# Kernel tuning notes

Hardware: AMD Instinct MI355X
Metric: run time of the kernel (lower is better)

Reference implementation:

```python
import jax, jax.numpy as jnp
import numpy as np

N, E, M, D = 100000, 50000, 1000000, 128  # vertices, hyperedges, incidences, hidden


def setup_inputs() -> dict:
    key = jax.random.key(0)
    ks = jax.random.split(key, 9)
    v = jax.random.normal(ks[0], (N, D), dtype=jnp.float32)
    e = jax.random.normal(ks[1], (E, D), dtype=jnp.float32)
    vidx = jax.random.randint(ks[2], (M,), 0, N)
    eidx = jax.random.randint(ks[3], (M,), 0, E)
    v_reg_weight = jax.random.uniform(ks[4], (M, 1), dtype=jnp.float32)
    e_reg_weight = jax.random.uniform(ks[5], (M, 1), dtype=jnp.float32)
    v_reg_sum = jnp.ones((N, 1), dtype=jnp.float32)
    e_reg_sum = jnp.ones((E, 1), dtype=jnp.float32)
    # learned parameters
    W_v2e = jax.random.normal(ks[6], (D, D), dtype=jnp.float32)
    W_e2v = jax.random.normal(ks[7], (D, D), dtype=jnp.float32)
    b_v = jnp.zeros((D,), dtype=jnp.float32)
    b_e = jnp.zeros((D,), dtype=jnp.float32)
    v_weight = jax.random.uniform(ks[8], (N, 1), dtype=jnp.float32)  # args.v_weight
    return dict(v=v, e=e, vidx=vidx, eidx=eidx,
                v_reg_weight=v_reg_weight, e_reg_weight=e_reg_weight,
                v_reg_sum=v_reg_sum, e_reg_sum=e_reg_sum,
                W_v2e=W_v2e, W_e2v=W_e2v, b_v=b_v, b_e=b_e, v_weight=v_weight)


def reference(v, e, vidx, eidx, v_reg_weight, e_reg_weight, v_reg_sum, e_reg_sum,
              W_v2e, W_e2v, b_v, b_e, v_weight):
    # v2e: dense transform, gather by vidx, reweight, scatter_add into edges
    ve = jax.nn.relu(v @ W_v2e + b_v)                      # [N, D]
    v_out = v * v_weight * 4.0                             # v_fac = 4
    msg_ve = (ve * v_weight)[vidx] * v_reg_weight          # [M, D]
    e_out = e + jax.ops.segment_sum(msg_ve, eidx, num_segments=E)
    e_out = e_out / e_reg_sum
    # e2v: dense transform, gather by eidx, reweight, scatter_add into vertices
    ev = jax.nn.relu(e_out @ W_e2v + b_e)                  # [E, D]
    msg_ev = (ev / 3.0)[eidx] * e_reg_weight               # [M, D]
    v_out = v_out + jax.ops.segment_sum(msg_ev, vidx, num_segments=N)
    v_out = v_out / v_reg_sum
    # is_last_mod=True: no dropout
    return v_out, e_out
```

## Files before the change

kernel.cpp:

```cpp
#include <hip/hip_runtime.h>
#include <cstddef>

#define DD 128
#define PART_ELEMS 4096
#define MAXB 256
#define MAXW 512
#define WT_LD 136

typedef __attribute__((ext_vector_type(8))) short bf16x8;
typedef __attribute__((ext_vector_type(4))) float f32x4;

__device__ __forceinline__ unsigned bf16pk(float x, float y) {
    unsigned a = __float_as_uint(x);
    unsigned b = __float_as_uint(y);
    a = (a + 0x7FFFu + ((a >> 16) & 1u)) >> 16;
    b = (b + 0x7FFFu + ((b >> 16) & 1u)) >> 16;
    return a | (b << 16);
}
__device__ __forceinline__ unsigned short bf16r(float x) {
    unsigned u = __float_as_uint(x);
    return (unsigned short)((u + 0x7FFFu + ((u >> 16) & 1u)) >> 16);
}
__device__ __forceinline__ float bflo(unsigned u) { return __uint_as_float(u << 16); }
__device__ __forceinline__ float bfhi(unsigned u) { return __uint_as_float(u & 0xFFFF0000u); }

__global__ __launch_bounds__(256)
void conv_w_kernel(const float* __restrict__ W0, const float* __restrict__ W1,
                   unsigned short* __restrict__ Wt0, unsigned short* __restrict__ Wt1,
                   int* __restrict__ bcur_e, int* __restrict__ bcur_v, int e_cap, int v_cap)
{
    int idx = blockIdx.x * 256 + threadIdx.x;
    int k = idx >> 7, c = idx & 127;
    Wt0[c * 128 + k] = bf16r(W0[idx]);
    Wt1[c * 128 + k] = bf16r(W1[idx]);
    if (blockIdx.x == 0) {
        bcur_e[threadIdx.x] = threadIdx.x * e_cap;
        bcur_v[threadIdx.x] = threadIdx.x * v_cap;
    }
}

__global__ __launch_bounds__(256)
void part2_kernel(const int* __restrict__ eidx, const int* __restrict__ vidx,
                  const float* __restrict__ vrw, const float* __restrict__ erw,
                  int* __restrict__ bcur_e, int* __restrict__ bcur_v,
                  int2* __restrict__ tmp_e, int2* __restrict__ tmp_v,
                  int M, int e_shift, int v_shift, int e_bk, int v_bk)
{
    __shared__ int lcnt_e[MAXB], lbase_e[MAXB], lcnt_v[MAXB], lbase_v[MAXB];
    const int t = threadIdx.x;
    const int base = blockIdx.x * PART_ELEMS;
    const int end = min(base + PART_ELEMS, M);

    if (t < e_bk) lcnt_e[t] = 0;
    if (t < v_bk) lcnt_v[t] = 0;
    __syncthreads();
    for (int j = base + t; j < end; j += 256) {
        atomicAdd(&lcnt_e[eidx[j] >> e_shift], 1);
        atomicAdd(&lcnt_v[vidx[j] >> v_shift], 1);
    }
    __syncthreads();
    if (t < e_bk) { int c = lcnt_e[t]; lbase_e[t] = c ? atomicAdd(&bcur_e[t], c) : 0; lcnt_e[t] = 0; }
    if (t < v_bk) { int c = lcnt_v[t]; lbase_v[t] = c ? atomicAdd(&bcur_v[t], c) : 0; lcnt_v[t] = 0; }
    __syncthreads();
    for (int j = base + t; j < end; j += 256) {
        int ei = eidx[j], vi = vidx[j];
        int wqe = (int)(vrw[j] * 32767.0f + 0.5f); wqe = wqe < 32767 ? wqe : 32767;
        int wqv = (int)(erw[j] * 32767.0f + 0.5f); wqv = wqv < 32767 ? wqv : 32767;
        int be = ei >> e_shift;
        int pe = lbase_e[be] + atomicAdd(&lcnt_e[be], 1);
        tmp_e[pe] = make_int2(ei | (wqe << 17), vi);
        int bv = vi >> v_shift;
        int pv = lbase_v[bv] + atomicAdd(&lcnt_v[bv], 1);
        tmp_v[pv] = make_int2(vi | (wqv << 17), ei);
    }
}

__global__ __launch_bounds__(256)
void fine2_kernel(const int2* __restrict__ tmp_e, const int* __restrict__ bcur_e,
                  int e_cap, int e_shift, int En, int e_bk,
                  int* __restrict__ e_start, unsigned* __restrict__ e_pack,
                  const int2* __restrict__ tmp_v, const int* __restrict__ bcur_v,
                  int v_cap, int v_shift, int Nn, int v_bk,
                  int* __restrict__ v_start, unsigned* __restrict__ v_pack, int M)
{
    __shared__ int lcnt[MAXW];
    __shared__ int lstart[MAXW];
    __shared__ int sdata[256];
    __shared__ int scnt[256];
    __shared__ int spbase;

    const int t = threadIdx.x;
    const int2* tmp; const int* bcur; int cap, shift, n, nb, b;
    int* start; unsigned* pack;
    if ((int)blockIdx.x < e_bk) {
        tmp = tmp_e; bcur = bcur_e; cap = e_cap; shift = e_shift; n = En; nb = e_bk;
        start = e_start; pack = e_pack; b = blockIdx.x;
    } else {
        tmp = tmp_v; bcur = bcur_v; cap = v_cap; shift = v_shift; n = Nn; nb = v_bk;
        start = v_start; pack = v_pack; b = blockIdx.x - e_bk;
    }

    int cnt_t = (t < nb) ? (bcur[t] - t * cap) : 0;
    scnt[t] = cnt_t;
    __syncthreads();
    int xx = cnt_t;
    for (int off = 1; off < 256; off <<= 1) {
        int y = (t >= off) ? scnt[t - off] : 0;
        __syncthreads();
        xx += y;
        scnt[t] = xx;
        __syncthreads();
    }
    if (t == b) spbase = xx - cnt_t;
    if (b == nb - 1 && t == 0) start[n] = M;
    __syncthreads();
    const int pbase = spbase;

    const int d0 = b << shift;
    const int width = min(1 << shift, n - d0);
    const int tbase = b * cap;
    const int nrec = bcur[b] - tbase;

    lcnt[t] = 0; lcnt[t + 256] = 0;
    __syncthreads();
    for (int j = t; j < nrec; j += 256)
        atomicAdd(&lcnt[(tmp[tbase + j].x & 0x1FFFF) - d0], 1);
    __syncthreads();
    int a = lcnt[2 * t], bb = lcnt[2 * t + 1];
    int s = a + bb;
    sdata[t] = s;
    __syncthreads();
    int x = s;
    for (int off = 1; off < 256; off <<= 1) {
        int y = (t >= off) ? sdata[t - off] : 0;
        __syncthreads();
        x += y;
        sdata[t] = x;
        __syncthreads();
    }
    int ex = x - s;
    lstart[2 * t] = ex;
    lstart[2 * t + 1] = ex + a;
    lcnt[2 * t] = 0; lcnt[2 * t + 1] = 0;
    __syncthreads();
    for (int i = t; i < width; i += 256)
        start[d0 + i] = pbase + lstart[i];
    for (int j = t; j < nrec; j += 256) {
        int2 r = tmp[tbase + j];
        int di = (r.x & 0x1FFFF) - d0;
        int pos = pbase + lstart[di] + atomicAdd(&lcnt[di], 1);
        pack[pos] = (unsigned)r.y | (((unsigned)r.x >> 17) << 17);
    }
}

template<bool V2E>
__global__ __launch_bounds__(256)
void gemm_mfma_kernel(const float* __restrict__ A, const unsigned short* __restrict__ Wtg,
                      const float* __restrict__ bias, const float* __restrict__ rowwt,
                      unsigned* __restrict__ outb, int nrows, float scale)
{
    __shared__ unsigned short Wt[128 * WT_LD];
    __shared__ unsigned short At[64 * WT_LD];

    const int t = threadIdx.x;
    const int row0 = blockIdx.x * 64;

    {
        int r = t >> 1, h = t & 1;
        const uint4* src = reinterpret_cast<const uint4*>(Wtg + r * 128 + h * 64);
        uint4* dst = reinterpret_cast<uint4*>(&Wt[r * WT_LD + h * 64]);
        #pragma unroll
        for (int i = 0; i < 8; ++i) dst[i] = src[i];
    }
    {
        int r = t >> 2, q = t & 3;
        int grow = row0 + r;
        uint4 o[4];
        if (grow < nrows) {
            const float4* src = reinterpret_cast<const float4*>(A + (size_t)grow * DD + q * 32);
            #pragma unroll
            for (int i = 0; i < 4; ++i) {
                float4 f0 = src[2 * i];
                float4 f1 = src[2 * i + 1];
                o[i].x = bf16pk(f0.x, f0.y);
                o[i].y = bf16pk(f0.z, f0.w);
                o[i].z = bf16pk(f1.x, f1.y);
                o[i].w = bf16pk(f1.z, f1.w);
            }
        } else {
            #pragma unroll
            for (int i = 0; i < 4; ++i) o[i] = make_uint4(0, 0, 0, 0);
        }
        uint4* dst = reinterpret_cast<uint4*>(&At[r * WT_LD + q * 32]);
        #pragma unroll
        for (int i = 0; i < 4; ++i) dst[i] = o[i];
    }
    __syncthreads();

    const int w  = t >> 6;
    const int l  = t & 63;
    const int lr = l & 15;
    const int lk = (l >> 4) * 8;

    f32x4 acc[8];
    #pragma unroll
    for (int i = 0; i < 8; ++i) acc[i] = 0.0f;

    const int arow = w * 16 + lr;
    #pragma unroll
    for (int ks = 0; ks < 4; ++ks) {
        bf16x8 af = *reinterpret_cast<const bf16x8*>(&At[arow * WT_LD + lk + ks * 32]);
        #pragma unroll
        for (int ct = 0; ct < 8; ++ct) {
            bf16x8 bfr = *reinterpret_cast<const bf16x8*>(&Wt[(ct * 16 + lr) * WT_LD + lk + ks * 32]);
            acc[ct] = __builtin_amdgcn_mfma_f32_16x16x32_bf16(af, bfr, acc[ct], 0, 0, 0);
        }
    }

    float bcol[8];
    #pragma unroll
    for (int ct = 0; ct < 8; ++ct) bcol[ct] = bias[ct * 16 + lr];
    #pragma unroll
    for (int r = 0; r < 4; ++r) {
        int rl = w * 16 + (l >> 4) * 4 + r;
        int grow = row0 + rl;
        float rw = scale;
        if (V2E) rw = (grow < nrows) ? rowwt[grow] : 0.f;
        #pragma unroll
        for (int ct = 0; ct < 8; ++ct) {
            float val = fmaxf(acc[ct][r] + bcol[ct], 0.f) * rw;
            At[rl * WT_LD + ct * 16 + lr] = bf16r(val);
        }
    }
    {
        int r = t >> 2, part = t & 3;
        int grow = row0 + r;
        if (grow < nrows) {
            const uint4* src = reinterpret_cast<const uint4*>(&At[r * WT_LD + part * 32]);
            uint4* dst = reinterpret_cast<uint4*>(outb + (size_t)grow * 64 + part * 16);
            dst[0] = src[0]; dst[1] = src[1]; dst[2] = src[2]; dst[3] = src[3];
        }
    }
}

__global__ __launch_bounds__(256)
void e_agg_kernel(const float* __restrict__ e, const unsigned* __restrict__ vwb,
                  const int* __restrict__ start, const unsigned* __restrict__ pack,
                  const float* __restrict__ ers, float* __restrict__ eout, int E)
{
    int row = blockIdx.x * 4 + (threadIdx.x >> 6);
    if (row >= E) return;
    int lane = threadIdx.x & 63;
    int half = lane >> 5;
    int sl = lane & 31;
    int s = start[row], t = start[row + 1];

    float a0 = 0.f, a1 = 0.f, a2 = 0.f, a3 = 0.f;
    float b0 = 0.f, b1 = 0.f, b2 = 0.f, b3 = 0.f;
    float c0 = 0.f, c1 = 0.f, c2 = 0.f, c3 = 0.f;
    float d0 = 0.f, d1 = 0.f, d2 = 0.f, d3 = 0.f;

    int j = s;
    for (; j + 8 <= t; j += 8) {
        unsigned pw0 = pack[j + half];
        unsigned pw1 = pack[j + 2 + half];
        unsigned pw2 = pack[j + 4 + half];
        unsigned pw3 = pack[j + 6 + half];
        uint2 u0 = *reinterpret_cast<const uint2*>(&vwb[(size_t)(pw0 & 0x1FFFFu) * 64 + sl * 2]);
        uint2 u1 = *reinterpret_cast<const uint2*>(&vwb[(size_t)(pw1 & 0x1FFFFu) * 64 + sl * 2]);
        uint2 u2 = *reinterpret_cast<const uint2*>(&vwb[(size_t)(pw2 & 0x1FFFFu) * 64 + sl * 2]);
        uint2 u3 = *reinterpret_cast<const uint2*>(&vwb[(size_t)(pw3 & 0x1FFFFu) * 64 + sl * 2]);
        float w0 = (float)(pw0 >> 17) * (1.0f / 32767.0f);
        float w1 = (float)(pw1 >> 17) * (1.0f / 32767.0f);
        float w2 = (float)(pw2 >> 17) * (1.0f / 32767.0f);
        float w3 = (float)(pw3 >> 17) * (1.0f / 32767.0f);
        a0 = fmaf(bflo(u0.x), w0, a0); a1 = fmaf(bfhi(u0.x), w0, a1);
        a2 = fmaf(bflo(u0.y), w0, a2); a3 = fmaf(bfhi(u0.y), w0, a3);
        b0 = fmaf(bflo(u1.x), w1, b0); b1 = fmaf(bfhi(u1.x), w1, b1);
        b2 = fmaf(bflo(u1.y), w1, b2); b3 = fmaf(bfhi(u1.y), w1, b3);
        c0 = fmaf(bflo(u2.x), w2, c0); c1 = fmaf(bfhi(u2.x), w2, c1);
        c2 = fmaf(bflo(u2.y), w2, c2); c3 = fmaf(bfhi(u2.y), w2, c3);
        d0 = fmaf(bflo(u3.x), w3, d0); d1 = fmaf(bfhi(u3.x), w3, d1);
        d2 = fmaf(bflo(u3.y), w3, d2); d3 = fmaf(bfhi(u3.y), w3, d3);
    }
    for (; j < t; j += 2) {
        int jj = j + half;
        if (jj < t) {
            unsigned pw = pack[jj];
            float wm = (float)(pw >> 17) * (1.0f / 32767.0f);
            uint2 u = *reinterpret_cast<const uint2*>(&vwb[(size_t)(pw & 0x1FFFFu) * 64 + sl * 2]);
            a0 = fmaf(bflo(u.x), wm, a0); a1 = fmaf(bfhi(u.x), wm, a1);
            a2 = fmaf(bflo(u.y), wm, a2); a3 = fmaf(bfhi(u.y), wm, a3);
        }
    }
    float s0 = (a0 + b0) + (c0 + d0);
    float s1 = (a1 + b1) + (c1 + d1);
    float s2 = (a2 + b2) + (c2 + d2);
    float s3 = (a3 + b3) + (c3 + d3);
    s0 += __shfl_xor(s0, 32, 64);
    s1 += __shfl_xor(s1, 32, 64);
    s2 += __shfl_xor(s2, 32, 64);
    s3 += __shfl_xor(s3, 32, 64);
    if (half == 0) {
        float rs = 1.0f / ers[row];
        float4 er = *reinterpret_cast<const float4*>(&e[(size_t)row * DD + sl * 4]);
        float4 o = make_float4((er.x + s0) * rs, (er.y + s1) * rs,
                               (er.z + s2) * rs, (er.w + s3) * rs);
        *reinterpret_cast<float4*>(&eout[(size_t)row * DD + sl * 4]) = o;
    }
}

__global__ __launch_bounds__(256)
void v_agg_kernel(const float* __restrict__ v, const unsigned* __restrict__ evb,
                  const int* __restrict__ start, const unsigned* __restrict__ pack,
                  const float* __restrict__ vrs, const float* __restrict__ vweight,
                  float* __restrict__ vout, int N)
{
    int row = blockIdx.x * 4 + (threadIdx.x >> 6);
    if (row >= N) return;
    int lane = threadIdx.x & 63;
    int half = lane >> 5;
    int sl = lane & 31;
    int s = start[row], t = start[row + 1];

    float a0 = 0.f, a1 = 0.f, a2 = 0.f, a3 = 0.f;
    float b0 = 0.f, b1 = 0.f, b2 = 0.f, b3 = 0.f;
    float c0 = 0.f, c1 = 0.f, c2 = 0.f, c3 = 0.f;
    float d0 = 0.f, d1 = 0.f, d2 = 0.f, d3 = 0.f;

    int j = s;
    for (; j + 8 <= t; j += 8) {
        unsigned pw0 = pack[j + half];
        unsigned pw1 = pack[j + 2 + half];
        unsigned pw2 = pack[j + 4 + half];
        unsigned pw3 = pack[j + 6 + half];
        uint2 u0 = *reinterpret_cast<const uint2*>(&evb[(size_t)(pw0 & 0x1FFFFu) * 64 + sl * 2]);
        uint2 u1 = *reinterpret_cast<const uint2*>(&evb[(size_t)(pw1 & 0x1FFFFu) * 64 + sl * 2]);
        uint2 u2 = *reinterpret_cast<const uint2*>(&evb[(size_t)(pw2 & 0x1FFFFu) * 64 + sl * 2]);
        uint2 u3 = *reinterpret_cast<const uint2*>(&evb[(size_t)(pw3 & 0x1FFFFu) * 64 + sl * 2]);
        float w0 = (float)(pw0 >> 17) * (1.0f / 32767.0f);
        float w1 = (float)(pw1 >> 17) * (1.0f / 32767.0f);
        float w2 = (float)(pw2 >> 17) * (1.0f / 32767.0f);
        float w3 = (float)(pw3 >> 17) * (1.0f / 32767.0f);
        a0 = fmaf(bflo(u0.x), w0, a0); a1 = fmaf(bfhi(u0.x), w0, a1);
        a2 = fmaf(bflo(u0.y), w0, a2); a3 = fmaf(bfhi(u0.y), w0, a3);
        b0 = fmaf(bflo(u1.x), w1, b0); b1 = fmaf(bfhi(u1.x), w1, b1);
        b2 = fmaf(bflo(u1.y), w1, b2); b3 = fmaf(bfhi(u1.y), w1, b3);
        c0 = fmaf(bflo(u2.x), w2, c0); c1 = fmaf(bfhi(u2.x), w2, c1);
        c2 = fmaf(bflo(u2.y), w2, c2); c3 = fmaf(bfhi(u2.y), w2, c3);
        d0 = fmaf(bflo(u3.x), w3, d0); d1 = fmaf(bfhi(u3.x), w3, d1);
        d2 = fmaf(bflo(u3.y), w3, d2); d3 = fmaf(bfhi(u3.y), w3, d3);
    }
    for (; j < t; j += 2) {
        int jj = j + half;
        if (jj < t) {
            unsigned pw = pack[jj];
            float wm = (float)(pw >> 17) * (1.0f / 32767.0f);
            uint2 u = *reinterpret_cast<const uint2*>(&evb[(size_t)(pw & 0x1FFFFu) * 64 + sl * 2]);
            a0 = fmaf(bflo(u.x), wm, a0); a1 = fmaf(bfhi(u.x), wm, a1);
            a2 = fmaf(bflo(u.y), wm, a2); a3 = fmaf(bfhi(u.y), wm, a3);
        }
    }
    float s0 = (a0 + b0) + (c0 + d0);
    float s1 = (a1 + b1) + (c1 + d1);
    float s2 = (a2 + b2) + (c2 + d2);
    float s3 = (a3 + b3) + (c3 + d3);
    s0 += __shfl_xor(s0, 32, 64);
    s1 += __shfl_xor(s1, 32, 64);
    s2 += __shfl_xor(s2, 32, 64);
    s3 += __shfl_xor(s3, 32, 64);
    if (half == 0) {
        float rs = 1.0f / vrs[row];
        float wt = vweight[row] * 4.0f;
        float4 vr = *reinterpret_cast<const float4*>(&v[(size_t)row * DD + sl * 4]);
        float4 o = make_float4((vr.x * wt + s0) * rs, (vr.y * wt + s1) * rs,
                               (vr.z * wt + s2) * rs, (vr.w * wt + s3) * rs);
        *reinterpret_cast<float4*>(&vout[(size_t)row * DD + sl * 4]) = o;
    }
}

extern "C" void kernel_launch(void* const* d_in, const int* in_sizes, int n_in,
                              void* d_out, int out_size, void* d_ws, size_t ws_size,
                              hipStream_t stream)
{
    const float* v       = (const float*)d_in[0];
    const float* e       = (const float*)d_in[1];
    const int*   vidx    = (const int*)d_in[2];
    const int*   eidx    = (const int*)d_in[3];
    const float* vrw     = (const float*)d_in[4];
    const float* erw     = (const float*)d_in[5];
    const float* vrs     = (const float*)d_in[6];
    const float* ers     = (const float*)d_in[7];
    const float* Wv2e    = (const float*)d_in[8];
    const float* We2v    = (const float*)d_in[9];
    const float* bv      = (const float*)d_in[10];
    const float* be      = (const float*)d_in[11];
    const float* vweight = (const float*)d_in[12];

    const int N = in_sizes[0] / DD;
    const int E = in_sizes[1] / DD;
    const int M = in_sizes[2];

    float* vout = (float*)d_out;
    float* eout = vout + (size_t)N * DD;

    auto calc_shift = [](int n) {
        int s = 0;
        while (((n + (1 << s) - 1) >> s) > MAXB) ++s;
        return s;
    };
    const int e_shift = calc_shift(E);
    const int v_shift = calc_shift(N);
    const int e_bk = (E + (1 << e_shift) - 1) >> e_shift;
    const int v_bk = (N + (1 << v_shift) - 1) >> v_shift;
    const int e_cap = ((M / e_bk) * 3) / 2 + 256;
    const int v_cap = ((M / v_bk) * 3) / 2 + 256;

    char* wsb = (char*)d_ws;
    size_t off = 0;
    auto alloc = [&](size_t bytes) { char* p = wsb + off; off += (bytes + 255) & ~(size_t)255; return p; };
    unsigned* vwb   = (unsigned*)alloc((size_t)N * 64 * sizeof(unsigned));
    unsigned* evb   = vwb;
    int*   e_start = (int*)alloc((size_t)(E + 1) * sizeof(int));
    int*   v_start = (int*)alloc((size_t)(N + 1) * sizeof(int));
    int*   bcur_e  = (int*)alloc(MAXB * sizeof(int));
    int*   bcur_v  = (int*)alloc(MAXB * sizeof(int));
    unsigned short* Wt0 = (unsigned short*)alloc(DD * DD * sizeof(unsigned short));
    unsigned short* Wt1 = (unsigned short*)alloc(DD * DD * sizeof(unsigned short));
    unsigned* e_pack = (unsigned*)alloc((size_t)M * sizeof(unsigned));
    unsigned* v_pack = (unsigned*)alloc((size_t)M * sizeof(unsigned));
    int2*  tmp_e   = (int2*)alloc((size_t)e_bk * e_cap * sizeof(int2));
    int2*  tmp_v   = (int2*)alloc((size_t)v_bk * v_cap * sizeof(int2));

    const int pblk = (M + PART_ELEMS - 1) / PART_ELEMS;

    conv_w_kernel<<<64, 256, 0, stream>>>(Wv2e, We2v, Wt0, Wt1, bcur_e, bcur_v, e_cap, v_cap);
    part2_kernel<<<pblk, 256, 0, stream>>>(eidx, vidx, vrw, erw, bcur_e, bcur_v,
                                           tmp_e, tmp_v, M, e_shift, v_shift, e_bk, v_bk);
    fine2_kernel<<<e_bk + v_bk, 256, 0, stream>>>(tmp_e, bcur_e, e_cap, e_shift, E, e_bk, e_start, e_pack,
                                                  tmp_v, bcur_v, v_cap, v_shift, N, v_bk, v_start, v_pack, M);
    gemm_mfma_kernel<true><<<(N + 63) / 64, 256, 0, stream>>>(v, Wt0, bv, vweight, vwb, N, 1.0f);
    e_agg_kernel<<<(E + 3) / 4, 256, 0, stream>>>(e, vwb, e_start, e_pack, ers, eout, E);
    gemm_mfma_kernel<false><<<(E + 63) / 64, 256, 0, stream>>>(eout, Wt1, be, nullptr, evb, E, 1.0f / 3.0f);
    v_agg_kernel<<<(N + 3) / 4, 256, 0, stream>>>(v, evb, v_start, v_pack, vrs, vweight, vout, N);
}
```

Measured before the change: 191.4 us.

## Merge fine sort with v2e GEMM launch and widen gather loads to 16 bytes

Combines the fine-bucket CSR construction and the vertex GEMM into one launch that picks its role from the block index and overlays their shared memory in a union, so the two independent stages can run concurrently instead of one after the other. The aggregation kernels now have each wavefront handle four incidences at a time with 16-byte bf16 row loads per lane, replacing two incidences with 8-byte loads. The partial sums are combined with two shuffle stages. This is meant to cut launch gaps and issue fewer, wider memory requests. The cost is higher register use and a larger shared-memory footprint for the fine blocks.

After: 181.7 us (median of 2 runs). 1.05x faster.

```diff
diff --git a/kernel.cpp b/kernel.cpp
--- a/kernel.cpp
+++ b/kernel.cpp
@@ -75,100 +75,95 @@
     }
 }
 
-__global__ __launch_bounds__(256)
-void fine2_kernel(const int2* __restrict__ tmp_e, const int* __restrict__ bcur_e,
-                  int e_cap, int e_shift, int En, int e_bk,
-                  int* __restrict__ e_start, unsigned* __restrict__ e_pack,
-                  const int2* __restrict__ tmp_v, const int* __restrict__ bcur_v,
-                  int v_cap, int v_shift, int Nn, int v_bk,
-                  int* __restrict__ v_start, unsigned* __restrict__ v_pack, int M)
-{
-    __shared__ int lcnt[MAXW];
-    __shared__ int lstart[MAXW];
-    __shared__ int sdata[256];
-    __shared__ int scnt[256];
-    __shared__ int spbase;
-
+struct FineLds { int lcnt[MAXW]; int lstart[MAXW]; int sdata[256]; int scnt[256]; int spbase; };
+struct GemmLds { unsigned short Wt[128 * WT_LD]; unsigned short At[64 * WT_LD]; };
+
+__device__ __forceinline__
+void fine_body(int blk, FineLds& L,
+               const int2* __restrict__ tmp_e, const int* __restrict__ bcur_e,
+               int e_cap, int e_shift, int En, int e_bk,
+               int* __restrict__ e_start, unsigned* __restrict__ e_pack,
+               const int2* __restrict__ tmp_v, const int* __restrict__ bcur_v,
+               int v_cap, int v_shift, int Nn, int v_bk,
+               int* __restrict__ v_start, unsigned* __restrict__ v_pack, int M)
+{
     const int t = threadIdx.x;
     const int2* tmp; const int* bcur; int cap, shift, n, nb, b;
     int* start; unsigned* pack;
-    if ((int)blockIdx.x < e_bk) {
+    if (blk < e_bk) {
         tmp = tmp_e; bcur = bcur_e; cap = e_cap; shift = e_shift; n = En; nb = e_bk;
-        start = e_start; pack = e_pack; b = blockIdx.x;
+        start = e_start; pack = e_pack; b = blk;
     } else {
         tmp = tmp_v; bcur = bcur_v; cap = v_cap; shift = v_shift; n = Nn; nb = v_bk;
-        start = v_start; pack = v_pack; b = blockIdx.x - e_bk;
+        start = v_start; pack = v_pack; b = blk - e_bk;
     }
 
     int cnt_t = (t < nb) ? (bcur[t] - t * cap) : 0;
-    scnt[t] = cnt_t;
+    L.scnt[t] = cnt_t;
     __syncthreads();
     int xx = cnt_t;
     for (int off = 1; off < 256; off <<= 1) {
-        int y = (t >= off) ? scnt[t - off] : 0;
+        int y = (t >= off) ? L.scnt[t - off] : 0;
         __syncthreads();
         xx += y;
-        scnt[t] = xx;
+        L.scnt[t] = xx;
         __syncthreads();
     }
-    if (t == b) spbase = xx - cnt_t;
+    if (t == b) L.spbase = xx - cnt_t;
     if (b == nb - 1 && t == 0) start[n] = M;
     __syncthreads();
-    const int pbase = spbase;
+    const int pbase = L.spbase;
 
     const int d0 = b << shift;
     const int width = min(1 << shift, n - d0);
     const int tbase = b * cap;
     const int nrec = bcur[b] - tbase;
 
-    lcnt[t] = 0; lcnt[t + 256] = 0;
+    L.lcnt[t] = 0; L.lcnt[t + 256] = 0;
     __syncthreads();
     for (int j = t; j < nrec; j += 256)
-        atomicAdd(&lcnt[(tmp[tbase + j].x & 0x1FFFF) - d0], 1);
-    __syncthreads();
-    int a = lcnt[2 * t], bb = lcnt[2 * t + 1];
+        atomicAdd(&L.lcnt[(tmp[tbase + j].x & 0x1FFFF) - d0], 1);
+    __syncthreads();
+    int a = L.lcnt[2 * t], bb = L.lcnt[2 * t + 1];
     int s = a + bb;
-    sdata[t] = s;
+    L.sdata[t] = s;
     __syncthreads();
     int x = s;
     for (int off = 1; off < 256; off <<= 1) {
-        int y = (t >= off) ? sdata[t - off] : 0;
+        int y = (t >= off) ? L.sdata[t - off] : 0;
         __syncthreads();
         x += y;
-        sdata[t] = x;
+        L.sdata[t] = x;
         __syncthreads();
     }
     int ex = x - s;
-    lstart[2 * t] = ex;
-    lstart[2 * t + 1] = ex + a;
-    lcnt[2 * t] = 0; lcnt[2 * t + 1] = 0;
+    L.lstart[2 * t] = ex;
+    L.lstart[2 * t + 1] = ex + a;
+    L.lcnt[2 * t] = 0; L.lcnt[2 * t + 1] = 0;
     __syncthreads();
     for (int i = t; i < width; i += 256)
-        start[d0 + i] = pbase + lstart[i];
+        start[d0 + i] = pbase + L.lstart[i];
     for (int j = t; j < nrec; j += 256) {
         int2 r = tmp[tbase + j];
         int di = (r.x & 0x1FFFF) - d0;
-        int pos = pbase + lstart[di] + atomicAdd(&lcnt[di], 1);
+        int pos = pbase + L.lstart[di] + atomicAdd(&L.lcnt[di], 1);
         pack[pos] = (unsigned)r.y | (((unsigned)r.x >> 17) << 17);
     }
 }
 
-template<bool V2E>
-__global__ __launch_bounds__(256)
-void gemm_mfma_kernel(const float* __restrict__ A, const unsigned short* __restrict__ Wtg,
-                      const float* __restrict__ bias, const float* __restrict__ rowwt,
-                      unsigned* __restrict__ outb, int nrows, float scale)
-{
-    __shared__ unsigned short Wt[128 * WT_LD];
-    __shared__ unsigned short At[64 * WT_LD];
-
+__device__ __forceinline__
+void gemm_body(int blk, GemmLds& L, const float* __restrict__ A,
+               const unsigned short* __restrict__ Wtg, const float* __restrict__ bias,
+               const float* __restrict__ rowwt, unsigned* __restrict__ outb,
+               int nrows, float scale, bool v2e)
+{
     const int t = threadIdx.x;
-    const int row0 = blockIdx.x * 64;
+    const int row0 = blk * 64;
 
     {
         int r = t >> 1, h = t & 1;
         const uint4* src = reinterpret_cast<const uint4*>(Wtg + r * 128 + h * 64);
-        uint4* dst = reinterpret_cast<uint4*>(&Wt[r * WT_LD + h * 64]);
+        uint4* dst = reinterpret_cast<uint4*>(&L.Wt[r * WT_LD + h * 64]);
         #pragma unroll
         for (int i = 0; i < 8; ++i) dst[i] = src[i];
     }
@@ -191,7 +186,7 @@
             #pragma unroll
             for (int i = 0; i < 4; ++i) o[i] = make_uint4(0, 0, 0, 0);
         }
-        uint4* dst = reinterpret_cast<uint4*>(&At[r * WT_LD + q * 32]);
+        uint4* dst = reinterpret_cast<uint4*>(&L.At[r * WT_LD + q * 32]);
         #pragma unroll
         for (int i = 0; i < 4; ++i) dst[i] = o[i];
     }
@@ -209,10 +204,10 @@
     const int arow = w * 16 + lr;
     #pragma unroll
     for (int ks = 0; ks < 4; ++ks) {
-        bf16x8 af = *reinterpret_cast<const bf16x8*>(&At[arow * WT_LD + lk + ks * 32]);
+        bf16x8 af = *reinterpret_cast<const bf16x8*>(&L.At[arow * WT_LD + lk + ks * 32]);
         #pragma unroll
         for (int ct = 0; ct < 8; ++ct) {
-            bf16x8 bfr = *reinterpret_cast<const bf16x8*>(&Wt[(ct * 16 + lr) * WT_LD + lk + ks * 32]);
+            bf16x8 bfr = *reinterpret_cast<const bf16x8*>(&L.Wt[(ct * 16 + lr) * WT_LD + lk + ks * 32]);
             acc[ct] = __builtin_amdgcn_mfma_f32_16x16x32_bf16(af, bfr, acc[ct], 0, 0, 0);
         }
     }
@@ -225,22 +220,52 @@
         int rl = w * 16 + (l >> 4) * 4 + r;
         int grow = row0 + rl;
         float rw = scale;
-        if (V2E) rw = (grow < nrows) ? rowwt[grow] : 0.f;
+        if (v2e) rw = (grow < nrows) ? rowwt[grow] : 0.f;
         #pragma unroll
         for (int ct = 0; ct < 8; ++ct) {
             float val = fmaxf(acc[ct][r] + bcol[ct], 0.f) * rw;
-            At[rl * WT_LD + ct * 16 + lr] = bf16r(val);
+            L.At[rl * WT_LD + ct * 16 + lr] = bf16r(val);
         }
     }
     {
         int r = t >> 2, part = t & 3;
         int grow = row0 + r;
         if (grow < nrows) {
-            const uint4* src = reinterpret_cast<const uint4*>(&At[r * WT_LD + part * 32]);
+            const uint4* src = reinterpret_cast<const uint4*>(&L.At[r * WT_LD + part * 32]);
             uint4* dst = reinterpret_cast<uint4*>(outb + (size_t)grow * 64 + part * 16);
             dst[0] = src[0]; dst[1] = src[1]; dst[2] = src[2]; dst[3] = src[3];
         }
     }
+}
+
+__global__ __launch_bounds__(256)
+void fused_fine_gemm_kernel(const int2* __restrict__ tmp_e, const int* __restrict__ bcur_e,
+                            int e_cap, int e_shift, int En, int e_bk,
+                            int* __restrict__ e_start, unsigned* __restrict__ e_pack,
+                            const int2* __restrict__ tmp_v, const int* __restrict__ bcur_v,
+                            int v_cap, int v_shift, int Nn, int v_bk,
+                            int* __restrict__ v_start, unsigned* __restrict__ v_pack, int M,
+                            const float* __restrict__ v, const unsigned short* __restrict__ Wt0,
+                            const float* __restrict__ bv, const float* __restrict__ vweight,
+                            unsigned* __restrict__ vwb)
+{
+    __shared__ union SM { FineLds f; GemmLds g; } sm;
+    const int nfine = e_bk + v_bk;
+    if ((int)blockIdx.x < nfine) {
+        fine_body(blockIdx.x, sm.f, tmp_e, bcur_e, e_cap, e_shift, En, e_bk, e_start, e_pack,
+                  tmp_v, bcur_v, v_cap, v_shift, Nn, v_bk, v_start, v_pack, M);
+    } else {
+        gemm_body(blockIdx.x - nfine, sm.g, v, Wt0, bv, vweight, vwb, Nn, 1.0f, true);
+    }
+}
+
+__global__ __launch_bounds__(256)
+void gemm_mfma_kernel(const float* __restrict__ A, const unsigned short* __restrict__ Wtg,
+                      const float* __restrict__ bias, unsigned* __restrict__ outb,
+                      int nrows, float scale)
+{
+    __shared__ GemmLds sm;
+    gemm_body(blockIdx.x, sm, A, Wtg, bias, nullptr, outb, nrows, scale, false);
 }
 
 __global__ __launch_bounds__(256)
@@ -251,62 +276,60 @@
     int row = blockIdx.x * 4 + (threadIdx.x >> 6);
     if (row >= E) return;
     int lane = threadIdx.x & 63;
-    int half = lane >> 5;
-    int sl = lane & 31;
+    int qw = lane >> 4;
+    int ql = lane & 15;
     int s = start[row], t = start[row + 1];
 
-    float a0 = 0.f, a1 = 0.f, a2 = 0.f, a3 = 0.f;
-    float b0 = 0.f, b1 = 0.f, b2 = 0.f, b3 = 0.f;
-    float c0 = 0.f, c1 = 0.f, c2 = 0.f, c3 = 0.f;
-    float d0 = 0.f, d1 = 0.f, d2 = 0.f, d3 = 0.f;
+    float a0=0.f,a1=0.f,a2=0.f,a3=0.f,a4=0.f,a5=0.f,a6=0.f,a7=0.f;
+    float b0=0.f,b1=0.f,b2=0.f,b3=0.f,b4=0.f,b5=0.f,b6=0.f,b7=0.f;
 
     int j = s;
     for (; j + 8 <= t; j += 8) {
-        unsigned pw0 = pack[j + half];
-        unsigned pw1 = pack[j + 2 + half];
-        unsigned pw2 = pack[j + 4 + half];
-        unsigned pw3 = pack[j + 6 + half];
-        uint2 u0 = *reinterpret_cast<const uint2*>(&vwb[(size_t)(pw0 & 0x1FFFFu) * 64 + sl * 2]);
-        uint2 u1 = *reinterpret_cast<const uint2*>(&vwb[(size_t)(pw1 & 0x1FFFFu) * 64 + sl * 2]);
-        uint2 u2 = *reinterpret_cast<const uint2*>(&vwb[(size_t)(pw2 & 0x1FFFFu) * 64 + sl * 2]);
-        uint2 u3 = *reinterpret_cast<const uint2*>(&vwb[(size_t)(pw3 & 0x1FFFFu) * 64 + sl * 2]);
+        unsigned pw0 = pack[j + qw];
+        unsigned pw1 = pack[j + 4 + qw];
+        uint4 u0 = *reinterpret_cast<const uint4*>(&vwb[(size_t)(pw0 & 0x1FFFFu) * 64 + ql * 4]);
+        uint4 u1 = *reinterpret_cast<const uint4*>(&vwb[(size_t)(pw1 & 0x1FFFFu) * 64 + ql * 4]);
         float w0 = (float)(pw0 >> 17) * (1.0f / 32767.0f);
         float w1 = (float)(pw1 >> 17) * (1.0f / 32767.0f);
-        float w2 = (float)(pw2 >> 17) * (1.0f / 32767.0f);
-        float w3 = (float)(pw3 >> 17) * (1.0f / 32767.0f);
         a0 = fmaf(bflo(u0.x), w0, a0); a1 = fmaf(bfhi(u0.x), w0, a1);
         a2 = fmaf(bflo(u0.y), w0, a2); a3 = fmaf(bfhi(u0.y), w0, a3);
+        a4 = fmaf(bflo(u0.z), w0, a4); a5 = fmaf(bfhi(u0.z), w0, a5);
+        a6 = fmaf(bflo(u0.w), w0, a6); a7 = fmaf(bfhi(u0.w), w0, a7);
         b0 = fmaf(bflo(u1.x), w1, b0); b1 = fmaf(bfhi(u1.x), w1, b1);
         b2 = fmaf(bflo(u1.y), w1, b2); b3 = fmaf(bfhi(u1.y), w1, b3);
-        c0 = fmaf(bflo(u2.x), w2, c0); c1 = fmaf(bfhi(u2.x), w2, c1);
-        c2 = fmaf(bflo(u2.y), w2, c2); c3 = fmaf(bfhi(u2.y), w2, c3);
-        d0 = fmaf(bflo(u3.x), w3, d0); d1 = fmaf(bfhi(u3.x), w3, d1);
-        d2 = fmaf(bflo(u3.y), w3, d2); d3 = fmaf(bfhi(u3.y), w3, d3);
-    }
-    for (; j < t; j += 2) {
-        int jj = j + half;
+        b4 = fmaf(bflo(u1.z), w1, b4); b5 = fmaf(bfhi(u1.z), w1, b5);
+        b6 = fmaf(bflo(u1.w), w1, b6); b7 = fmaf(bfhi(u1.w), w1, b7);
+    }
+    for (; j < t; j += 4) {
+        int jj = j + qw;
         if (jj < t) {
             unsigned pw = pack[jj];
             float wm = (float)(pw >> 17) * (1.0f / 32767.0f);
-            uint2 u = *reinterpret_cast<const uint2*>(&vwb[(size_t)(pw & 0x1FFFFu) * 64 + sl * 2]);
+            uint4 u = *reinterpret_cast<const uint4*>(&vwb[(size_t)(pw & 0x1FFFFu) * 64 + ql * 4]);
             a0 = fmaf(bflo(u.x), wm, a0); a1 = fmaf(bfhi(u.x), wm, a1);
             a2 = fmaf(bflo(u.y), wm, a2); a3 = fmaf(bfhi(u.y), wm, a3);
-        }
-    }
-    float s0 = (a0 + b0) + (c0 + d0);
-    float s1 = (a1 + b1) + (c1 + d1);
-    float s2 = (a2 + b2) + (c2 + d2);
-    float s3 = (a3 + b3) + (c3 + d3);
-    s0 += __shfl_xor(s0, 32, 64);
-    s1 += __shfl_xor(s1, 32, 64);
-    s2 += __shfl_xor(s2, 32, 64);
-    s3 += __shfl_xor(s3, 32, 64);
-    if (half == 0) {
+            a4 = fmaf(bflo(u.z), wm, a4); a5 = fmaf(bfhi(u.z), wm, a5);
+            a6 = fmaf(bflo(u.w), wm, a6); a7 = fmaf(bfhi(u.w), wm, a7);
+        }
+    }
+    float r0 = a0 + b0, r1 = a1 + b1, r2 = a2 + b2, r3 = a3 + b3;
+    float r4 = a4 + b4, r5 = a5 + b5, r6 = a6 + b6, r7 = a7 + b7;
+    r0 += __shfl_xor(r0, 16, 64); r0 += __shfl_xor(r0, 32, 64);
+    r1 += __shfl_xor(r1, 16, 64); r1 += __shfl_xor(r1, 32, 64);
+    r2 += __shfl_xor(r2, 16, 64); r2 += __shfl_xor(r2, 32, 64);
+    r3 += __shfl_xor(r3, 16, 64); r3 += __shfl_xor(r3, 32, 64);
+    r4 += __shfl_xor(r4, 16, 64); r4 += __shfl_xor(r4, 32, 64);
+    r5 += __shfl_xor(r5, 16, 64); r5 += __shfl_xor(r5, 32, 64);
+    r6 += __shfl_xor(r6, 16, 64); r6 += __shfl_xor(r6, 32, 64);
+    r7 += __shfl_xor(r7, 16, 64); r7 += __shfl_xor(r7, 32, 64);
+    if (qw == 0) {
         float rs = 1.0f / ers[row];
-        float4 er = *reinterpret_cast<const float4*>(&e[(size_t)row * DD + sl * 4]);
-        float4 o = make_float4((er.x + s0) * rs, (er.y + s1) * rs,
-                               (er.z + s2) * rs, (er.w + s3) * rs);
-        *reinterpret_cast<float4*>(&eout[(size_t)row * DD + sl * 4]) = o;
+        const float4* ep = reinterpret_cast<const float4*>(&e[(size_t)row * DD + ql * 8]);
+        float4 e0 = ep[0], e1 = ep[1];
+        float4 o0 = make_float4((e0.x + r0) * rs, (e0.y + r1) * rs, (e0.z + r2) * rs, (e0.w + r3) * rs);
+        float4 o1 = make_float4((e1.x + r4) * rs, (e1.y + r5) * rs, (e1.z + r6) * rs, (e1.w + r7) * rs);
+        float4* op = reinterpret_cast<float4*>(&eout[(size_t)row * DD + ql * 8]);
+        op[0] = o0; op[1] = o1;
     }
 }
 
@@ -319,63 +342,63 @@
     int row = blockIdx.x * 4 + (threadIdx.x >> 6);
     if (row >= N) return;
     int lane = threadIdx.x & 63;
-    int half = lane >> 5;
-    int sl = lane & 31;
+    int qw = lane >> 4;
+    int ql = lane & 15;
     int s = start[row], t = start[row + 1];
 
-    float a0 = 0.f, a1 = 0.f, a2 = 0.f, a3 = 0.f;
-    float b0 = 0.f, b1 = 0.f, b2 = 0.f, b3 = 0.f;
-    float c0 = 0.f, c1 = 0.f, c2 = 0.f, c3 = 0.f;
-    float d0 = 0.f, d1 = 0.f, d2 = 0.f, d3 = 0.f;
+    float a0=0.f,a1=0.f,a2=0.f,a3=0.f,a4=0.f,a5=0.f,a6=0.f,a7=0.f;
+    float b0=0.f,b1=0.f,b2=0.f,b3=0.f,b4=0.f,b5=0.f,b6=0.f,b7=0.f;
 
     int j = s;
     for (; j + 8 <= t; j += 8) {
-        unsigned pw0 = pack[j + half];
-        unsigned pw1 = pack[j + 2 + half];
-        unsigned pw2 = pack[j + 4 + half];
-        unsigned pw3 = pack[j + 6 + half];
-        uint2 u0 = *reinterpret_cast<const uint2*>(&evb[(size_t)(pw0 & 0x1FFFFu) * 64 + sl * 2]);
-        uint2 u1 = *reinterpret_cast<const uint2*>(&evb[(size_t)(pw1 & 0x1FFFFu) * 64 + sl * 2]);
-        uint2 u2 = *reinterpret_cast<const uint2*>(&evb[(size_t)(pw2 & 0x1FFFFu) * 64 + sl * 2]);
-        uint2 u3 = *reinterpret_cast<const uint2*>(&evb[(size_t)(pw3 & 0x1FFFFu) * 64 + sl * 2]);
+        unsigned pw0 = pack[j + qw];
+        unsigned pw1 = pack[j + 4 + qw];
+        uint4 u0 = *reinterpret_cast<const uint4*>(&evb[(size_t)(pw0 & 0x1FFFFu) * 64 + ql * 4]);
+        uint4 u1 = *reinterpret_cast<const uint4*>(&evb[(size_t)(pw1 & 0x1FFFFu) * 64 + ql * 4]);
         float w0 = (float)(pw0 >> 17) * (1.0f / 32767.0f);
         float w1 = (float)(pw1 >> 17) * (1.0f / 32767.0f);
-        float w2 = (float)(pw2 >> 17) * (1.0f / 32767.0f);
-        float w3 = (float)(pw3 >> 17) * (1.0f / 32767.0f);
         a0 = fmaf(bflo(u0.x), w0, a0); a1 = fmaf(bfhi(u0.x), w0, a1);
         a2 = fmaf(bflo(u0.y), w0, a2); a3 = fmaf(bfhi(u0.y), w0, a3);
+        a4 = fmaf(bflo(u0.z), w0, a4); a5 = fmaf(bfhi(u0.z), w0, a5);
+        a6 = fmaf(bflo(u0.w), w0, a6); a7 = fmaf(bfhi(u0.w), w0, a7);
         b0 = fmaf(bflo(u1.x), w1, b0); b1 = fmaf(bfhi(u1.x), w1, b1);
         b2 = fmaf(bflo(u1.y), w1, b2); b3 = fmaf(bfhi(u1.y), w1, b3);
-        c0 = fmaf(bflo(u2.x), w2, c0); c1 = fmaf(bfhi(u2.x), w2, c1);
-        c2 = fmaf(bflo(u2.y), w2, c2); c3 = fmaf(bfhi(u2.y), w2, c3);
-        d0 = fmaf(bflo(u3.x), w3, d0); d1 = fmaf(bfhi(u3.x), w3, d1);
-        d2 = fmaf(bflo(u3.y), w3, d2); d3 = fmaf(bfhi(u3.y), w3, d3);
-    }
-    for (; j < t; j += 2) {
-        int jj = j + half;
+        b4 = fmaf(bflo(u1.z), w1, b4); b5 = fmaf(bfhi(u1.z), w1, b5);
+        b6 = fmaf(bflo(u1.w), w1, b6); b7 = fmaf(bfhi(u1.w), w1, b7);
+    }
+    for (; j < t; j += 4) {
+        int jj = j + qw;
         if (jj < t) {
             unsigned pw = pack[jj];
             float wm = (float)(pw >> 17) * (1.0f / 32767.0f);
-            uint2 u = *reinterpret_cast<const uint2*>(&evb[(size_t)(pw & 0x1FFFFu) * 64 + sl * 2]);
+            uint4 u = *reinterpret_cast<const uint4*>(&evb[(size_t)(pw & 0x1FFFFu) * 64 + ql * 4]);
             a0 = fmaf(bflo(u.x), wm, a0); a1 = fmaf(bfhi(u.x), wm, a1);
             a2 = fmaf(bflo(u.y), wm, a2); a3 = fmaf(bfhi(u.y), wm, a3);
-        }
-    }
-    float s0 = (a0 + b0) + (c0 + d0);
-    float s1 = (a1 + b1) + (c1 + d1);
-    float s2 = (a2 + b2) + (c2 + d2);
-    float s3 = (a3 + b3) + (c3 + d3);
-    s0 += __shfl_xor(s0, 32, 64);
-    s1 += __shfl_xor(s1, 32, 64);
-    s2 += __shfl_xor(s2, 32, 64);
-    s3 += __shfl_xor(s3, 32, 64);
-    if (half == 0) {
+            a4 = fmaf(bflo(u.z), wm, a4); a5 = fmaf(bfhi(u.z), wm, a5);
+            a6 = fmaf(bflo(u.w), wm, a6); a7 = fmaf(bfhi(u.w), wm, a7);
+        }
+    }
+    float r0 = a0 + b0, r1 = a1 + b1, r2 = a2 + b2, r3 = a3 + b3;
+    float r4 = a4 + b4, r5 = a5 + b5, r6 = a6 + b6, r7 = a7 + b7;
+    r0 += __shfl_xor(r0, 16, 64); r0 += __shfl_xor(r0, 32, 64);
+    r1 += __shfl_xor(r1, 16, 64); r1 += __shfl_xor(r1, 32, 64);
+    r2 += __shfl_xor(r2, 16, 64); r2 += __shfl_xor(r2, 32, 64);
+    r3 += __shfl_xor(r3, 16, 64); r3 += __shfl_xor(r3, 32, 64);
+    r4 += __shfl_xor(r4, 16, 64); r4 += __shfl_xor(r4, 32, 64);
+    r5 += __shfl_xor(r5, 16, 64); r5 += __shfl_xor(r5, 32, 64);
+    r6 += __shfl_xor(r6, 16, 64); r6 += __shfl_xor(r6, 32, 64);
+    r7 += __shfl_xor(r7, 16, 64); r7 += __shfl_xor(r7, 32, 64);
+    if (qw == 0) {
         float rs = 1.0f / vrs[row];
         float wt = vweight[row] * 4.0f;
-        float4 vr = *reinterpret_cast<const float4*>(&v[(size_t)row * DD + sl * 4]);
-        float4 o = make_float4((vr.x * wt + s0) * rs, (vr.y * wt + s1) * rs,
-                               (vr.z * wt + s2) * rs, (vr.w * wt + s3) * rs);
-        *reinterpret_cast<float4*>(&vout[(size_t)row * DD + sl * 4]) = o;
+        const float4* vp = reinterpret_cast<const float4*>(&v[(size_t)row * DD + ql * 8]);
+        float4 v0 = vp[0], v1 = vp[1];
+        float4 o0 = make_float4((v0.x * wt + r0) * rs, (v0.y * wt + r1) * rs,
+                                (v0.z * wt + r2) * rs, (v0.w * wt + r3) * rs);
+        float4 o1 = make_float4((v1.x * wt + r4) * rs, (v1.y * wt + r5) * rs,
+                                (v1.z * wt + r6) * rs, (v1.w * wt + r7) * rs);
+        float4* op = reinterpret_cast<float4*>(&vout[(size_t)row * DD + ql * 8]);
+        op[0] = o0; op[1] = o1;
     }
 }
 
@@ -433,14 +456,16 @@
     int2*  tmp_v   = (int2*)alloc((size_t)v_bk * v_cap * sizeof(int2));
 
     const int pblk = (M + PART_ELEMS - 1) / PART_ELEMS;
+    const int gblkN = (N + 63) / 64;
 
     conv_w_kernel<<<64, 256, 0, stream>>>(Wv2e, We2v, Wt0, Wt1, bcur_e, bcur_v, e_cap, v_cap);
     part2_kernel<<<pblk, 256, 0, stream>>>(eidx, vidx, vrw, erw, bcur_e, bcur_v,
                                            tmp_e, tmp_v, M, e_shift, v_shift, e_bk, v_bk);
-    fine2_kernel<<<e_bk + v_bk, 256, 0, stream>>>(tmp_e, bcur_e, e_cap, e_shift, E, e_bk, e_start, e_pack,
-                                                  tmp_v, bcur_v, v_cap, v_shift, N, v_bk, v_start, v_pack, M);
-    gemm_mfma_kernel<true><<<(N + 63) / 64, 256, 0, stream>>>(v, Wt0, bv, vweight, vwb, N, 1.0f);
+    fused_fine_gemm_kernel<<<e_bk + v_bk + gblkN, 256, 0, stream>>>(
+        tmp_e, bcur_e, e_cap, e_shift, E, e_bk, e_start, e_pack,
+        tmp_v, bcur_v, v_cap, v_shift, N, v_bk, v_start, v_pack, M,
+        v, Wt0, bv, vweight, vwb);
     e_agg_kernel<<<(E + 3) / 4, 256, 0, stream>>>(e, vwb, e_start, e_pack, ers, eout, E);
-    gemm_mfma_kernel<false><<<(E + 63) / 64, 256, 0, stream>>>(eout, Wt1, be, nullptr, evb, E, 1.0f / 3.0f);
+    gemm_mfma_kernel<<<(E + 63) / 64, 256, 0, stream>>>(eout, Wt1, be, evb, E, 1.0f / 3.0f);
     v_agg_kernel<<<(N + 3) / 4, 256, 0, stream>>>(v, evb, v_start, v_pack, vrs, vweight, vout, N);
 }
```
